# Kernel optimization log

Hardware: AMD Instinct MI355X
Metric: run time of the kernel (lower is better)

Reference implementation:

```python
import jax, jax.numpy as jnp
import numpy as np

B, C, D = 131072, 256, 64
STEPS, DT, BETA, EPS = 8, 0.15, 1.0, 1e-4


def setup_inputs() -> dict:
    key = jax.random.key(0)
    k1, k2 = jax.random.split(key)
    z = jax.random.normal(k1, (B, D), dtype=jnp.float32)
    centers = jax.random.normal(k2, (C, D), dtype=jnp.float32) * 0.7
    mus = jnp.ones((C,), dtype=jnp.float32) * 0.5
    return {"z": z, "centers": centers, "mus": mus}


def reference(z, centers, mus):
    # |z - c|^2 = |z|^2 + |c|^2 - 2 z.c  (exact same math as the per-center loop,
    # vectorized over all centers; the rvec sum g = -sum_c mu_c (z - c)/r^3
    # factorizes into two matmuls: w @ centers - z * sum(w)).
    cn2 = jnp.sum(centers * centers, axis=1)  # [C]

    def body(zc, _):
        zz = jnp.sum(zc * zc, axis=1, keepdims=True)              # [B,1]
        r2 = jnp.maximum(zz + cn2[None, :] - 2.0 * (zc @ centers.T), 0.0) + EPS  # [B,C]
        r = jnp.sqrt(r2)                                          # [B,C]
        n = 1.0 + jnp.sum(mus / r, axis=1)                        # [B]
        w = mus / (r2 * r)                                        # mu / r^3, [B,C]
        g = (w @ centers - zc * jnp.sum(w, axis=1, keepdims=True)) / n[:, None]
        znew = jnp.clip(zc + DT * BETA * g, -3.0, 3.0)
        return znew, None

    zf, _ = jax.lax.scan(body, z, None, length=STEPS)
    return zf
```

## Files before the change

kernel.cpp:

```cpp
#include <hip/hip_runtime.h>


#define STEPS 8
#define DTB   0.15f
#define EPSF  1e-4f

typedef short bf16x8 __attribute__((ext_vector_type(8)));
typedef float f32x4  __attribute__((ext_vector_type(4)));
typedef float f32x2  __attribute__((ext_vector_type(2)));
union FragU { int4 i; bf16x8 h; };

__device__ __forceinline__ f32x2 max2(f32x2 a, f32x2 b) {
    return __builtin_elementwise_max(a, b);
}
__device__ __forceinline__ f32x2 min2(f32x2 a, f32x2 b) {
    return __builtin_elementwise_min(a, b);
}

__device__ __forceinline__ unsigned bfpt(float lo, float hi) {
    return __builtin_amdgcn_perm(__float_as_uint(hi), __float_as_uint(lo),
                                 0x07060302u);
}
__device__ __forceinline__ unsigned bfp(float lo, float hi) {
    return __builtin_amdgcn_perm(__float_as_uint(hi) + 0x8000u,
                                 __float_as_uint(lo) + 0x8000u, 0x07060302u);
}

__global__ void pm_prep(const float* __restrict__ centers,
                        const float* __restrict__ mus,
                        unsigned* __restrict__ ws) {
    const int gtid = blockIdx.x * 256 + threadIdx.x;
    if (gtid < 2048) {
        const int c = gtid >> 9, Mt = (gtid >> 7) & 3, h = (gtid >> 6) & 1;
        const int L = gtid & 63, m16 = L & 15, q = L >> 4;
        const float* row = centers + (size_t)(64 * c + 16 * Mt + m16) * 64 + 32 * h + 8 * q;
        uint4 u;
        u.x = bfp(-2.f * row[0], -2.f * row[1]);
        u.y = bfp(-2.f * row[2], -2.f * row[3]);
        u.z = bfp(-2.f * row[4], -2.f * row[5]);
        u.w = bfp(-2.f * row[6], -2.f * row[7]);
        ((uint4*)ws)[gtid] = u;
    } else if (gtid < 4096) {
        const int i = gtid - 2048;
        const int Mt = i >> 9, c = (i >> 7) & 3, h = (i >> 6) & 1;
        const int L = i & 63, m16 = L & 15, q = L >> 4;
        const float* base = centers + (size_t)(64 * c + 32 * h + 8 * q) * 64 + 16 * Mt + m16;
        uint4 u;
        u.x = bfp(base[0],   base[64]);
        u.y = bfp(base[128], base[192]);
        u.z = bfp(base[256], base[320]);
        u.w = bfp(base[384], base[448]);
        ((uint4*)ws)[gtid] = u;
    } else if (gtid < 4352) {
        const int t = gtid - 4096;
        const float* r = centers + (size_t)t * 64;
        float a0 = 0.f, a1 = 0.f, a2 = 0.f, a3 = 0.f;
#pragma unroll
        for (int d = 0; d < 64; d += 4) {
            a0 = fmaf(r[d],     r[d],     a0);
            a1 = fmaf(r[d + 1], r[d + 1], a1);
            a2 = fmaf(r[d + 2], r[d + 2], a2);
            a3 = fmaf(r[d + 3], r[d + 3], a3);
        }
        float c2 = (a0 + a1) + (a2 + a3);
        ((float*)ws)[16384 + t] = c2;
        ((float*)ws)[16640 + t] = mus[t];
    }
}

__global__ __launch_bounds__(256, 2)
void pm_main(const float* __restrict__ z_in,
             const unsigned* __restrict__ ws,
             float* __restrict__ z_out) {
    __shared__ int4 sA[2048];
    __shared__ int4 sWF[4][4][64];

    const int4* wsA = (const int4*)ws;
    const int4* wsG = wsA + 2048;
    const float* wsC  = (const float*)ws + 16384;
    const float* wsMu = (const float*)ws + 16640;

    const int tid  = threadIdx.x;
    const int lane = tid & 63;
    const int w    = tid >> 6;
    const int m16  = lane & 15;
    const int q    = lane >> 4;

#pragma unroll
    for (int i = 0; i < 8; ++i) sA[i * 256 + tid] = wsA[i * 256 + tid];
    __syncthreads();

    const int pbase = blockIdx.x * 128;

    f32x4 z[4][2];
#pragma unroll
    for (int Mt = 0; Mt < 4; ++Mt)
#pragma unroll
        for (int Nt = 0; Nt < 2; ++Nt)
            z[Mt][Nt] = *(const f32x4*)(z_in + (size_t)(pbase + 32 * w + m16 + 16 * Nt) * 64
                                        + 16 * Mt + 4 * q);

    unsigned* wp = (unsigned*)&sWF[w][0][0];

#pragma unroll 1
    for (int s = 0; s < STEPS; ++s) {
        float zzp[2];
#pragma unroll
        for (int Nt = 0; Nt < 2; ++Nt) {
            f32x2 a2 = (f32x2){0.f, 0.f};
#pragma unroll
            for (int Mt = 0; Mt < 4; ++Mt) {
                f32x2 lo = (f32x2){z[Mt][Nt][0], z[Mt][Nt][1]};
                f32x2 hi = (f32x2){z[Mt][Nt][2], z[Mt][Nt][3]};
                a2 += lo * lo;
                a2 += hi * hi;
            }
            float a = a2.x + a2.y;
            a += __shfl_xor(a, 16, 64);
            a += __shfl_xor(a, 32, 64);
            zzp[Nt] = a;
        }

#pragma unroll
        for (int Mt = 0; Mt < 4; ++Mt) {
            const int Kt = Mt >> 1;
            const int qt = (2 * Mt + (q >> 1)) & 3;
#pragma unroll
            for (int Nt = 0; Nt < 2; ++Nt) {
                const int pos = ((Kt * 2 + Nt) * 64 + m16 + 16 * qt) * 4 + 2 * (q & 1);
                *(uint2*)(wp + pos) = make_uint2(bfp(z[Mt][Nt][0], z[Mt][Nt][1]),
                                                 bfp(z[Mt][Nt][2], z[Mt][Nt][3]));
            }
        }
        FragU zf[2][2];
#pragma unroll
        for (int Kt = 0; Kt < 2; ++Kt)
#pragma unroll
            for (int Nt = 0; Nt < 2; ++Nt)
                zf[Kt][Nt].i = sWF[w][Kt * 2 + Nt][lane];

        f32x4 g[4][2];
#pragma unroll
        for (int Mt = 0; Mt < 4; ++Mt)
#pragma unroll
            for (int Nt = 0; Nt < 2; ++Nt) g[Mt][Nt] = (f32x4){0.f, 0.f, 0.f, 0.f};
        f32x2 nacc2[2] = {(f32x2){0.f, 0.f}, (f32x2){0.f, 0.f}};
        f32x2 swp2[2]  = {(f32x2){0.f, 0.f}, (f32x2){0.f, 0.f}};

#pragma unroll 1
        for (int c = 0; c < 4; ++c) {
#pragma unroll
            for (int Mt = 0; Mt < 4; ++Mt) {
                FragU a0, a1;
                a0.i = sA[((c * 4 + Mt) * 2 + 0) * 64 + lane];
                a1.i = sA[((c * 4 + Mt) * 2 + 1) * 64 + lane];
                const float4 cn4 = *(const float4*)(wsC  + 64 * c + 16 * Mt + 4 * q);
                const float4 mu4 = *(const float4*)(wsMu + 64 * c + 16 * Mt + 4 * q);
                const f32x2 cnlo = (f32x2){cn4.x, cn4.y}, cnhi = (f32x2){cn4.z, cn4.w};
                const f32x2 mulo = (f32x2){mu4.x, mu4.y}, muhi = (f32x2){mu4.z, mu4.w};
                f32x4 S[2];
#pragma unroll
                for (int Nt = 0; Nt < 2; ++Nt) {
                    const f32x2 zz2 = (f32x2){zzp[Nt], zzp[Nt]};
                    const f32x2 i0 = zz2 + cnlo, i1 = zz2 + cnhi;
                    f32x4 acc = (f32x4){i0.x, i0.y, i1.x, i1.y};
                    acc = __builtin_amdgcn_mfma_f32_16x16x32_bf16(a0.h, zf[0][Nt].h, acc, 0, 0, 0);
                    acc = __builtin_amdgcn_mfma_f32_16x16x32_bf16(a1.h, zf[1][Nt].h, acc, 0, 0, 0);
                    S[Nt] = acc;
                }

                const int Kt = Mt >> 1;
                const int qt = (2 * Mt + (q >> 1)) & 3;
                const f32x2 eps2 = (f32x2){EPSF, EPSF};
#pragma unroll
                for (int Nt = 0; Nt < 2; ++Nt) {
                    f32x2 s0 = (f32x2){S[Nt][0], S[Nt][1]};
                    f32x2 s1 = (f32x2){S[Nt][2], S[Nt][3]};
                    f32x2 r20 = max2(s0, eps2);
                    f32x2 r21 = max2(s1, eps2);
                    f32x2 rin0, rin1;
                    rin0.x = __builtin_amdgcn_rsqf(r20.x);
                    rin0.y = __builtin_amdgcn_rsqf(r20.y);
                    rin1.x = __builtin_amdgcn_rsqf(r21.x);
                    rin1.y = __builtin_amdgcn_rsqf(r21.y);
                    f32x2 mur0 = mulo * rin0, mur1 = muhi * rin1;
                    nacc2[Nt] += mur0;
                    nacc2[Nt] += mur1;
                    f32x2 q0 = rin0 * rin0, q1 = rin1 * rin1;
                    f32x2 wv0 = mur0 * q0,  wv1 = mur1 * q1;
                    swp2[Nt] += wv0;
                    swp2[Nt] += wv1;
                    const int pos = ((Kt * 2 + Nt) * 64 + m16 + 16 * qt) * 4 + 2 * (q & 1);
                    *(uint2*)(wp + pos) = make_uint2(bfpt(wv0.x, wv0.y),
                                                     bfpt(wv1.x, wv1.y));
                }
            }

            FragU wf[2][2];
#pragma unroll
            for (int Kt = 0; Kt < 2; ++Kt)
#pragma unroll
                for (int Nt = 0; Nt < 2; ++Nt)
                    wf[Kt][Nt].i = sWF[w][Kt * 2 + Nt][lane];
#pragma unroll
            for (int Mt = 0; Mt < 4; ++Mt) {
                FragU ga0, ga1;
                ga0.i = wsG[((Mt * 4 + c) * 2 + 0) * 64 + lane];
                ga1.i = wsG[((Mt * 4 + c) * 2 + 1) * 64 + lane];
#pragma unroll
                for (int Nt = 0; Nt < 2; ++Nt) {
                    g[Mt][Nt] = __builtin_amdgcn_mfma_f32_16x16x32_bf16(ga0.h, wf[0][Nt].h, g[Mt][Nt], 0, 0, 0);
                    g[Mt][Nt] = __builtin_amdgcn_mfma_f32_16x16x32_bf16(ga1.h, wf[1][Nt].h, g[Mt][Nt], 0, 0, 0);
                }
            }
        }

        float tco[2], swf[2];
#pragma unroll
        for (int Nt = 0; Nt < 2; ++Nt) {
            float a = nacc2[Nt].x + nacc2[Nt].y;
            a += __shfl_xor(a, 16, 64);
            a += __shfl_xor(a, 32, 64);
            float b = swp2[Nt].x + swp2[Nt].y;
            b += __shfl_xor(b, 16, 64);
            b += __shfl_xor(b, 32, 64);
            tco[Nt] = DTB * __builtin_amdgcn_rcpf(1.f + a);
            swf[Nt] = b;
        }
        const f32x2 lo2 = (f32x2){-3.f, -3.f}, hi2 = (f32x2){3.f, 3.f};
#pragma unroll
        for (int Mt = 0; Mt < 4; ++Mt)
#pragma unroll
            for (int Nt = 0; Nt < 2; ++Nt) {
                const f32x2 sw2 = (f32x2){swf[Nt], swf[Nt]};
                const f32x2 tc2 = (f32x2){tco[Nt], tco[Nt]};
#pragma unroll
                for (int p = 0; p < 2; ++p) {
                    f32x2 zp = (f32x2){z[Mt][Nt][2 * p], z[Mt][Nt][2 * p + 1]};
                    f32x2 gp = (f32x2){g[Mt][Nt][2 * p], g[Mt][Nt][2 * p + 1]};
                    f32x2 gd = gp - sw2 * zp;
                    f32x2 zn = zp + tc2 * gd;
                    zn = min2(max2(zn, lo2), hi2);
                    z[Mt][Nt][2 * p]     = zn.x;
                    z[Mt][Nt][2 * p + 1] = zn.y;
                }
            }
    }

#pragma unroll
    for (int Mt = 0; Mt < 4; ++Mt)
#pragma unroll
        for (int Nt = 0; Nt < 2; ++Nt)
            *(f32x4*)(z_out + (size_t)(pbase + 32 * w + m16 + 16 * Nt) * 64
                      + 16 * Mt + 4 * q) = z[Mt][Nt];
}

extern "C" void kernel_launch(void* const* d_in, const int* in_sizes, int n_in,
                              void* d_out, int out_size, void* d_ws, size_t ws_size,
                              hipStream_t stream) {
    const float* z       = (const float*)d_in[0];
    const float* centers = (const float*)d_in[1];
    const float* mus     = (const float*)d_in[2];
    float* out           = (float*)d_out;
    unsigned* ws         = (unsigned*)d_ws;

    pm_prep<<<dim3(17), dim3(256), 0, stream>>>(centers, mus, ws);
    pm_main<<<dim3(1024), dim3(256), 0, stream>>>(z, ws, out);
}
```

Baseline: 211.8 us.

## Double-buffer per-wave weight staging to overlap S-phase with G MFMAs

Enlarges the per-wave LDS staging buffer to two slots and software-pipelines the center-chunk loop. The S-phase (distance MFMAs plus rsqrt weights) for chunk c+1 is issued between loading chunk c's weight fragments and its gradient MFMAs. The goal is to let MFMA work on one chunk overlap with VALU/transcendental work on the next and hide LDS and global fragment-load latency. The cost is more LDS per block and higher register pressure from holding ga/wf fragments across the S-phase, which could hurt occupancy at 2 blocks per CU.

```diff
diff --git a/kernel.cpp b/kernel.cpp
--- a/kernel.cpp
+++ b/kernel.cpp
@@ -68,12 +68,80 @@
     }
 }
 
+#define S_PHASE(c_, wpu_)                                                      \
+  {                                                                            \
+    const f32x2 eps2 = (f32x2){EPSF, EPSF};                                    \
+    _Pragma("unroll")                                                          \
+    for (int Mt = 0; Mt < 4; ++Mt) {                                           \
+      FragU a0, a1;                                                            \
+      a0.i = sA[(((c_) * 4 + Mt) * 2 + 0) * 64 + lane];                        \
+      a1.i = sA[(((c_) * 4 + Mt) * 2 + 1) * 64 + lane];                        \
+      const float4 cn4 = *(const float4*)(wsC  + 64 * (c_) + 16 * Mt + 4 * q); \
+      const float4 mu4 = *(const float4*)(wsMu + 64 * (c_) + 16 * Mt + 4 * q); \
+      const f32x2 cnlo = (f32x2){cn4.x, cn4.y}, cnhi = (f32x2){cn4.z, cn4.w};  \
+      const f32x2 mulo = (f32x2){mu4.x, mu4.y}, muhi = (f32x2){mu4.z, mu4.w};  \
+      f32x4 S[2];                                                              \
+      _Pragma("unroll")                                                        \
+      for (int Nt = 0; Nt < 2; ++Nt) {                                         \
+        const f32x2 zz2 = (f32x2){zzp[Nt], zzp[Nt]};                           \
+        const f32x2 i0 = zz2 + cnlo, i1 = zz2 + cnhi;                          \
+        f32x4 acc = (f32x4){i0.x, i0.y, i1.x, i1.y};                           \
+        acc = __builtin_amdgcn_mfma_f32_16x16x32_bf16(a0.h, zf[0][Nt].h, acc, 0, 0, 0); \
+        acc = __builtin_amdgcn_mfma_f32_16x16x32_bf16(a1.h, zf[1][Nt].h, acc, 0, 0, 0); \
+        S[Nt] = acc;                                                           \
+      }                                                                        \
+      const int Kt = Mt >> 1;                                                  \
+      const int qt = (2 * Mt + (q >> 1)) & 3;                                  \
+      _Pragma("unroll")                                                        \
+      for (int Nt = 0; Nt < 2; ++Nt) {                                         \
+        f32x2 s0 = (f32x2){S[Nt][0], S[Nt][1]};                                \
+        f32x2 s1 = (f32x2){S[Nt][2], S[Nt][3]};                                \
+        f32x2 r20 = max2(s0, eps2);                                            \
+        f32x2 r21 = max2(s1, eps2);                                            \
+        f32x2 rin0, rin1;                                                      \
+        rin0.x = __builtin_amdgcn_rsqf(r20.x);                                 \
+        rin0.y = __builtin_amdgcn_rsqf(r20.y);                                 \
+        rin1.x = __builtin_amdgcn_rsqf(r21.x);                                 \
+        rin1.y = __builtin_amdgcn_rsqf(r21.y);                                 \
+        f32x2 mur0 = mulo * rin0, mur1 = muhi * rin1;                          \
+        nacc2[Nt] += mur0; nacc2[Nt] += mur1;                                  \
+        f32x2 q0 = rin0 * rin0, q1 = rin1 * rin1;                              \
+        f32x2 wv0 = mur0 * q0,  wv1 = mur1 * q1;                               \
+        swp2[Nt] += wv0; swp2[Nt] += wv1;                                      \
+        const int pos = ((Kt * 2 + Nt) * 64 + m16 + 16 * qt) * 4 + 2 * (q & 1);\
+        *(uint2*)((wpu_) + pos) = make_uint2(bfpt(wv0.x, wv0.y),               \
+                                             bfpt(wv1.x, wv1.y));              \
+      }                                                                        \
+    }                                                                          \
+  }
+
+#define G_LOAD(c_, wfb_)                                                       \
+  _Pragma("unroll")                                                            \
+  for (int Kt = 0; Kt < 2; ++Kt)                                               \
+    _Pragma("unroll")                                                          \
+    for (int Nt = 0; Nt < 2; ++Nt)                                             \
+      wf[Kt][Nt].i = (wfb_)[(Kt * 2 + Nt) * 64 + lane];                        \
+  _Pragma("unroll")                                                            \
+  for (int Mt = 0; Mt < 4; ++Mt) {                                             \
+    ga[Mt][0].i = wsG[((Mt * 4 + (c_)) * 2 + 0) * 64 + lane];                  \
+    ga[Mt][1].i = wsG[((Mt * 4 + (c_)) * 2 + 1) * 64 + lane];                  \
+  }
+
+#define G_MFMA()                                                               \
+  _Pragma("unroll")                                                            \
+  for (int Mt = 0; Mt < 4; ++Mt)                                               \
+    _Pragma("unroll")                                                          \
+    for (int Nt = 0; Nt < 2; ++Nt) {                                           \
+      g[Mt][Nt] = __builtin_amdgcn_mfma_f32_16x16x32_bf16(ga[Mt][0].h, wf[0][Nt].h, g[Mt][Nt], 0, 0, 0); \
+      g[Mt][Nt] = __builtin_amdgcn_mfma_f32_16x16x32_bf16(ga[Mt][1].h, wf[1][Nt].h, g[Mt][Nt], 0, 0, 0); \
+    }
+
 __global__ __launch_bounds__(256, 2)
 void pm_main(const float* __restrict__ z_in,
              const unsigned* __restrict__ ws,
              float* __restrict__ z_out) {
     __shared__ int4 sA[2048];
-    __shared__ int4 sWF[4][4][64];
+    __shared__ int4 sWF[4][8][64];
 
     const int4* wsA = (const int4*)ws;
     const int4* wsG = wsA + 2048;
@@ -100,7 +168,7 @@
             z[Mt][Nt] = *(const f32x4*)(z_in + (size_t)(pbase + 32 * w + m16 + 16 * Nt) * 64
                                         + 16 * Mt + 4 * q);
 
-    unsigned* wp = (unsigned*)&sWF[w][0][0];
+    int4* const wavebuf = &sWF[w][0][0];
 
 #pragma unroll 1
     for (int s = 0; s < STEPS; ++s) {
@@ -121,15 +189,18 @@
             zzp[Nt] = a;
         }
 
-#pragma unroll
-        for (int Mt = 0; Mt < 4; ++Mt) {
-            const int Kt = Mt >> 1;
-            const int qt = (2 * Mt + (q >> 1)) & 3;
-#pragma unroll
-            for (int Nt = 0; Nt < 2; ++Nt) {
-                const int pos = ((Kt * 2 + Nt) * 64 + m16 + 16 * qt) * 4 + 2 * (q & 1);
-                *(uint2*)(wp + pos) = make_uint2(bfp(z[Mt][Nt][0], z[Mt][Nt][1]),
-                                                 bfp(z[Mt][Nt][2], z[Mt][Nt][3]));
+        {
+            unsigned* zstage = (unsigned*)(wavebuf + 4 * 64);
+#pragma unroll
+            for (int Mt = 0; Mt < 4; ++Mt) {
+                const int Kt = Mt >> 1;
+                const int qt = (2 * Mt + (q >> 1)) & 3;
+#pragma unroll
+                for (int Nt = 0; Nt < 2; ++Nt) {
+                    const int pos = ((Kt * 2 + Nt) * 64 + m16 + 16 * qt) * 4 + 2 * (q & 1);
+                    *(uint2*)(zstage + pos) = make_uint2(bfp(z[Mt][Nt][0], z[Mt][Nt][1]),
+                                                         bfp(z[Mt][Nt][2], z[Mt][Nt][3]));
+                }
             }
         }
         FragU zf[2][2];
@@ -137,7 +208,7 @@
         for (int Kt = 0; Kt < 2; ++Kt)
 #pragma unroll
             for (int Nt = 0; Nt < 2; ++Nt)
-                zf[Kt][Nt].i = sWF[w][Kt * 2 + Nt][lane];
+                zf[Kt][Nt].i = wavebuf[4 * 64 + (Kt * 2 + Nt) * 64 + lane];
 
         f32x4 g[4][2];
 #pragma unroll
@@ -147,72 +218,22 @@
         f32x2 nacc2[2] = {(f32x2){0.f, 0.f}, (f32x2){0.f, 0.f}};
         f32x2 swp2[2]  = {(f32x2){0.f, 0.f}, (f32x2){0.f, 0.f}};
 
+        S_PHASE(0, (unsigned*)wavebuf)
+
 #pragma unroll 1
-        for (int c = 0; c < 4; ++c) {
-#pragma unroll
-            for (int Mt = 0; Mt < 4; ++Mt) {
-                FragU a0, a1;
-                a0.i = sA[((c * 4 + Mt) * 2 + 0) * 64 + lane];
-                a1.i = sA[((c * 4 + Mt) * 2 + 1) * 64 + lane];
-                const float4 cn4 = *(const float4*)(wsC  + 64 * c + 16 * Mt + 4 * q);
-                const float4 mu4 = *(const float4*)(wsMu + 64 * c + 16 * Mt + 4 * q);
-                const f32x2 cnlo = (f32x2){cn4.x, cn4.y}, cnhi = (f32x2){cn4.z, cn4.w};
-                const f32x2 mulo = (f32x2){mu4.x, mu4.y}, muhi = (f32x2){mu4.z, mu4.w};
-                f32x4 S[2];
-#pragma unroll
-                for (int Nt = 0; Nt < 2; ++Nt) {
-                    const f32x2 zz2 = (f32x2){zzp[Nt], zzp[Nt]};
-                    const f32x2 i0 = zz2 + cnlo, i1 = zz2 + cnhi;
-                    f32x4 acc = (f32x4){i0.x, i0.y, i1.x, i1.y};
-                    acc = __builtin_amdgcn_mfma_f32_16x16x32_bf16(a0.h, zf[0][Nt].h, acc, 0, 0, 0);
-                    acc = __builtin_amdgcn_mfma_f32_16x16x32_bf16(a1.h, zf[1][Nt].h, acc, 0, 0, 0);
-                    S[Nt] = acc;
-                }
-
-                const int Kt = Mt >> 1;
-                const int qt = (2 * Mt + (q >> 1)) & 3;
-                const f32x2 eps2 = (f32x2){EPSF, EPSF};
-#pragma unroll
-                for (int Nt = 0; Nt < 2; ++Nt) {
-                    f32x2 s0 = (f32x2){S[Nt][0], S[Nt][1]};
-                    f32x2 s1 = (f32x2){S[Nt][2], S[Nt][3]};
-                    f32x2 r20 = max2(s0, eps2);
-                    f32x2 r21 = max2(s1, eps2);
-                    f32x2 rin0, rin1;
-                    rin0.x = __builtin_amdgcn_rsqf(r20.x);
-                    rin0.y = __builtin_amdgcn_rsqf(r20.y);
-                    rin1.x = __builtin_amdgcn_rsqf(r21.x);
-                    rin1.y = __builtin_amdgcn_rsqf(r21.y);
-                    f32x2 mur0 = mulo * rin0, mur1 = muhi * rin1;
-                    nacc2[Nt] += mur0;
-                    nacc2[Nt] += mur1;
-                    f32x2 q0 = rin0 * rin0, q1 = rin1 * rin1;
-                    f32x2 wv0 = mur0 * q0,  wv1 = mur1 * q1;
-                    swp2[Nt] += wv0;
-                    swp2[Nt] += wv1;
-                    const int pos = ((Kt * 2 + Nt) * 64 + m16 + 16 * qt) * 4 + 2 * (q & 1);
-                    *(uint2*)(wp + pos) = make_uint2(bfpt(wv0.x, wv0.y),
-                                                     bfpt(wv1.x, wv1.y));
-                }
-            }
-
-            FragU wf[2][2];
-#pragma unroll
-            for (int Kt = 0; Kt < 2; ++Kt)
-#pragma unroll
-                for (int Nt = 0; Nt < 2; ++Nt)
-                    wf[Kt][Nt].i = sWF[w][Kt * 2 + Nt][lane];
-#pragma unroll
-            for (int Mt = 0; Mt < 4; ++Mt) {
-                FragU ga0, ga1;
-                ga0.i = wsG[((Mt * 4 + c) * 2 + 0) * 64 + lane];
-                ga1.i = wsG[((Mt * 4 + c) * 2 + 1) * 64 + lane];
-#pragma unroll
-                for (int Nt = 0; Nt < 2; ++Nt) {
-                    g[Mt][Nt] = __builtin_amdgcn_mfma_f32_16x16x32_bf16(ga0.h, wf[0][Nt].h, g[Mt][Nt], 0, 0, 0);
-                    g[Mt][Nt] = __builtin_amdgcn_mfma_f32_16x16x32_bf16(ga1.h, wf[1][Nt].h, g[Mt][Nt], 0, 0, 0);
-                }
-            }
+        for (int c = 0; c < 3; ++c) {
+            int4* bufA = wavebuf + (c & 1) * (4 * 64);
+            unsigned* bufB = (unsigned*)(wavebuf + ((c + 1) & 1) * (4 * 64));
+            FragU wf[2][2], ga[4][2];
+            G_LOAD(c, bufA)
+            S_PHASE(c + 1, bufB)
+            G_MFMA()
+        }
+        {
+            int4* bufA = wavebuf + 1 * (4 * 64);
+            FragU wf[2][2], ga[4][2];
+            G_LOAD(3, bufA)
+            G_MFMA()
         }
 
         float tco[2], swf[2];
```

After: 217.4 us. +2.6%, slower.

## Permute K dimension so MFMA outputs feed next MFMA directly in registers

Applied to the files above, without the earlier changes.

Reorders the feature dimension mapping (for z loads/stores and the prepacked center operand) so that the accumulator layout of one MFMA matches the B-operand fragment layout of the next. This removes the per-step and per-chunk LDS round trip (write to sWF, read back) for both z and the weight fragments, dropping the shared buffer. It relies on a consistent permutation between prep and main kernels; a mismatch would give wrong results.

```diff
diff --git a/kernel.cpp b/kernel.cpp
--- a/kernel.cpp
+++ b/kernel.cpp
@@ -44,12 +44,14 @@
         const int i = gtid - 2048;
         const int Mt = i >> 9, c = (i >> 7) & 3, h = (i >> 6) & 1;
         const int L = i & 63, m16 = L & 15, q = L >> 4;
-        const float* base = centers + (size_t)(64 * c + 32 * h + 8 * q) * 64 + 16 * Mt + m16;
+        const int dim = 32 * (Mt >> 1) + 8 * (m16 >> 2) + 4 * (Mt & 1) + (m16 & 3);
+        const float* b0 = centers + (size_t)(64 * c + 32 * h + 4 * q) * 64 + dim;
+        const float* b1 = b0 + 16 * 64;
         uint4 u;
-        u.x = bfp(base[0],   base[64]);
-        u.y = bfp(base[128], base[192]);
-        u.z = bfp(base[256], base[320]);
-        u.w = bfp(base[384], base[448]);
+        u.x = bfp(b0[0],   b0[64]);
+        u.y = bfp(b0[128], b0[192]);
+        u.z = bfp(b1[0],   b1[64]);
+        u.w = bfp(b1[128], b1[192]);
         ((uint4*)ws)[gtid] = u;
     } else if (gtid < 4352) {
         const int t = gtid - 4096;
@@ -73,7 +75,6 @@
              const unsigned* __restrict__ ws,
              float* __restrict__ z_out) {
     __shared__ int4 sA[2048];
-    __shared__ int4 sWF[4][4][64];
 
     const int4* wsA = (const int4*)ws;
     const int4* wsG = wsA + 2048;
@@ -98,9 +99,7 @@
 #pragma unroll
         for (int Nt = 0; Nt < 2; ++Nt)
             z[Mt][Nt] = *(const f32x4*)(z_in + (size_t)(pbase + 32 * w + m16 + 16 * Nt) * 64
-                                        + 16 * Mt + 4 * q);
-
-    unsigned* wp = (unsigned*)&sWF[w][0][0];
+                                        + 32 * (Mt >> 1) + 8 * q + 4 * (Mt & 1));
 
 #pragma unroll 1
     for (int s = 0; s < STEPS; ++s) {
@@ -121,23 +120,16 @@
             zzp[Nt] = a;
         }
 
-#pragma unroll
-        for (int Mt = 0; Mt < 4; ++Mt) {
-            const int Kt = Mt >> 1;
-            const int qt = (2 * Mt + (q >> 1)) & 3;
+        FragU zf[2][2];
+#pragma unroll
+        for (int Kt = 0; Kt < 2; ++Kt)
 #pragma unroll
             for (int Nt = 0; Nt < 2; ++Nt) {
-                const int pos = ((Kt * 2 + Nt) * 64 + m16 + 16 * qt) * 4 + 2 * (q & 1);
-                *(uint2*)(wp + pos) = make_uint2(bfp(z[Mt][Nt][0], z[Mt][Nt][1]),
-                                                 bfp(z[Mt][Nt][2], z[Mt][Nt][3]));
-            }
-        }
-        FragU zf[2][2];
-#pragma unroll
-        for (int Kt = 0; Kt < 2; ++Kt)
-#pragma unroll
-            for (int Nt = 0; Nt < 2; ++Nt)
-                zf[Kt][Nt].i = sWF[w][Kt * 2 + Nt][lane];
+                zf[Kt][Nt].i.x = (int)bfp(z[2 * Kt][Nt][0],     z[2 * Kt][Nt][1]);
+                zf[Kt][Nt].i.y = (int)bfp(z[2 * Kt][Nt][2],     z[2 * Kt][Nt][3]);
+                zf[Kt][Nt].i.z = (int)bfp(z[2 * Kt + 1][Nt][0], z[2 * Kt + 1][Nt][1]);
+                zf[Kt][Nt].i.w = (int)bfp(z[2 * Kt + 1][Nt][2], z[2 * Kt + 1][Nt][3]);
+            }
 
         f32x4 g[4][2];
 #pragma unroll
@@ -149,6 +141,8 @@
 
 #pragma unroll 1
         for (int c = 0; c < 4; ++c) {
+            FragU wfB[2][2];
+            const f32x2 eps2 = (f32x2){EPSF, EPSF};
 #pragma unroll
             for (int Mt = 0; Mt < 4; ++Mt) {
                 FragU a0, a1;
@@ -169,9 +163,6 @@
                     S[Nt] = acc;
                 }
 
-                const int Kt = Mt >> 1;
-                const int qt = (2 * Mt + (q >> 1)) & 3;
-                const f32x2 eps2 = (f32x2){EPSF, EPSF};
 #pragma unroll
                 for (int Nt = 0; Nt < 2; ++Nt) {
                     f32x2 s0 = (f32x2){S[Nt][0], S[Nt][1]};
@@ -190,18 +181,16 @@
                     f32x2 wv0 = mur0 * q0,  wv1 = mur1 * q1;
                     swp2[Nt] += wv0;
                     swp2[Nt] += wv1;
-                    const int pos = ((Kt * 2 + Nt) * 64 + m16 + 16 * qt) * 4 + 2 * (q & 1);
-                    *(uint2*)(wp + pos) = make_uint2(bfpt(wv0.x, wv0.y),
-                                                     bfpt(wv1.x, wv1.y));
-                }
-            }
-
-            FragU wf[2][2];
-#pragma unroll
-            for (int Kt = 0; Kt < 2; ++Kt)
-#pragma unroll
-                for (int Nt = 0; Nt < 2; ++Nt)
-                    wf[Kt][Nt].i = sWF[w][Kt * 2 + Nt][lane];
+                    if ((Mt & 1) == 0) {
+                        wfB[Mt >> 1][Nt].i.x = (int)bfpt(wv0.x, wv0.y);
+                        wfB[Mt >> 1][Nt].i.y = (int)bfpt(wv1.x, wv1.y);
+                    } else {
+                        wfB[Mt >> 1][Nt].i.z = (int)bfpt(wv0.x, wv0.y);
+                        wfB[Mt >> 1][Nt].i.w = (int)bfpt(wv1.x, wv1.y);
+                    }
+                }
+            }
+
 #pragma unroll
             for (int Mt = 0; Mt < 4; ++Mt) {
                 FragU ga0, ga1;
@@ -209,8 +198,8 @@
                 ga1.i = wsG[((Mt * 4 + c) * 2 + 1) * 64 + lane];
 #pragma unroll
                 for (int Nt = 0; Nt < 2; ++Nt) {
-                    g[Mt][Nt] = __builtin_amdgcn_mfma_f32_16x16x32_bf16(ga0.h, wf[0][Nt].h, g[Mt][Nt], 0, 0, 0);
-                    g[Mt][Nt] = __builtin_amdgcn_mfma_f32_16x16x32_bf16(ga1.h, wf[1][Nt].h, g[Mt][Nt], 0, 0, 0);
+                    g[Mt][Nt] = __builtin_amdgcn_mfma_f32_16x16x32_bf16(ga0.h, wfB[0][Nt].h, g[Mt][Nt], 0, 0, 0);
+                    g[Mt][Nt] = __builtin_amdgcn_mfma_f32_16x16x32_bf16(ga1.h, wfB[1][Nt].h, g[Mt][Nt], 0, 0, 0);
                 }
             }
         }
@@ -252,7 +241,7 @@
 #pragma unroll
         for (int Nt = 0; Nt < 2; ++Nt)
             *(f32x4*)(z_out + (size_t)(pbase + 32 * w + m16 + 16 * Nt) * 64
-                      + 16 * Mt + 4 * q) = z[Mt][Nt];
+                      + 32 * (Mt >> 1) + 8 * q + 4 * (Mt & 1)) = z[Mt][Nt];
 }
 
 extern "C" void kernel_launch(void* const* d_in, const int* in_sizes, int n_in,
```

After: 206.0 us. -2.7%, faster.
